# Performance work log

Measured on AMD Instinct MI355X. Metric: run time of the kernel, lower is better.

The kernel has to match this reference:

```python
import jax, jax.numpy as jnp
import numpy as np

D_MODEL = 1024
N_HEADS = 16
D_K = D_MODEL // N_HEADS


def setup_inputs() -> dict:
    key = jax.random.key(0)
    ks = jax.random.split(key, 16)
    B, S = 2, 2048
    sc = 1.0 / np.sqrt(D_MODEL)
    inp = {
        "query": jax.random.normal(ks[0], (B, S, D_MODEL), jnp.float32),
        "key": jax.random.normal(ks[1], (B, S, D_MODEL), jnp.float32),
        "value": jax.random.normal(ks[2], (B, S, D_MODEL), jnp.float32),
        "Wq": jax.random.normal(ks[3], (D_MODEL, D_MODEL), jnp.float32) * sc,
        "bq": jnp.zeros((D_MODEL,), jnp.float32),
        "Wk": jax.random.normal(ks[4], (D_MODEL, D_MODEL), jnp.float32) * sc,
        "bk": jnp.zeros((D_MODEL,), jnp.float32),
        "Wv": jax.random.normal(ks[5], (D_MODEL, D_MODEL), jnp.float32) * sc,
        "bv": jnp.zeros((D_MODEL,), jnp.float32),
        "Wo": jax.random.normal(ks[6], (D_MODEL, D_MODEL), jnp.float32) * sc,
        "bo": jnp.zeros((D_MODEL,), jnp.float32),
        "theta": jax.random.normal(ks[7], (N_HEADS,), jnp.float32) * 0.1,
        "gate": jax.random.normal(ks[8], (D_MODEL,), jnp.float32) * 0.1,
    }
    return inp


def reference(query, key, value, Wq, bq, Wk, bk, Wv, bv, Wo, bo, theta, gate):
    B, Sq, D = query.shape
    Sk = key.shape[1]
    # linear projections (torch Linear: x @ W.T + b), split heads -> [B,H,S,d_k]
    Q = (query @ Wq.T + bq).reshape(B, Sq, N_HEADS, D_K).transpose(0, 2, 1, 3)
    K = (key @ Wk.T + bk).reshape(B, Sk, N_HEADS, D_K).transpose(0, 2, 1, 3)
    V = (value @ Wv.T + bv).reshape(B, Sk, N_HEADS, D_K).transpose(0, 2, 1, 3)

    inv_sqrt_dk = 1.0 / jnp.sqrt(jnp.float32(D_K))
    scores = jnp.einsum("bhqd,bhkd->bhqk", Q, K) * inv_sqrt_dk

    # per-head rotation of the first two feature dims of Q
    cos_t = jnp.cos(theta)[None, :, None, None]  # [1,H,1,1]
    sin_t = jnp.sin(theta)[None, :, None, None]
    q_rot = jnp.concatenate(
        [
            cos_t * Q[..., :1] - sin_t * Q[..., 1:2],
            sin_t * Q[..., :1] + cos_t * Q[..., 1:2],
            Q[..., 2:],
        ],
        axis=-1,
    )
    scores_q = jnp.einsum("bhqd,bhkd->bhqk", q_rot, K) * inv_sqrt_dk

    g_scalar = jax.nn.sigmoid(gate.mean())
    scores = g_scalar * scores_q + (1.0 - g_scalar) * scores

    attn = jax.nn.softmax(scores, axis=-1)
    out = jnp.einsum("bhqk,bhkd->bhqd", attn, V)
    out = out.transpose(0, 2, 1, 3).reshape(B, Sq, D)
    return out @ Wo.T + bo
```

## Files before the change

kernel.cpp:

```cpp
#include <hip/hip_runtime.h>


typedef __bf16 bf16;
typedef __attribute__((ext_vector_type(8))) bf16 bf16x8;
typedef __attribute__((ext_vector_type(4))) bf16 bf16x4;
typedef __attribute__((ext_vector_type(2))) bf16 bf16x2;
typedef __attribute__((ext_vector_type(4))) float f32x4;
typedef unsigned int u32;

#define D_MODEL 1024
#define NH 16
#define DKH 64
#define SEQ 2048

#define GLL16(g, l) __builtin_amdgcn_global_load_lds(                      \
    (const __attribute__((address_space(1))) void*)(g),                    \
    (__attribute__((address_space(3))) void*)(l), 16, 0, 0)

static __device__ __forceinline__ f32x4 mfma16(bf16x8 a, bf16x8 b, f32x4 c) {
  return __builtin_amdgcn_mfma_f32_16x16x32_bf16(a, b, c, 0, 0, 0);
}

static __device__ __forceinline__ u32 pk2(float a, float b) {
  bf16x2 v; v[0] = (bf16)a; v[1] = (bf16)b;
  return __builtin_bit_cast(u32, v);
}

static __device__ __forceinline__ float fexp2(float x) {
#if __has_builtin(__builtin_amdgcn_exp2f)
  return __builtin_amdgcn_exp2f(x);
#else
  return exp2f(x);
#endif
}

#define CQK 0.1803368801111244f
#define MSHIFT 12.0f

__global__ __launch_bounds__(256) void prep(const float* __restrict__ query,
                                            const float* __restrict__ key,
                                            const float* __restrict__ value,
                                            const float* __restrict__ Wq,
                                            const float* __restrict__ bq,
                                            const float* __restrict__ Wk,
                                            const float* __restrict__ Wv,
                                            const float* __restrict__ Wo,
                                            const float* __restrict__ gate,
                                            const float* __restrict__ theta,
                                            bf16* __restrict__ Xq,
                                            bf16* __restrict__ Xk,
                                            bf16* __restrict__ Xv,
                                            bf16* __restrict__ Wqp,
                                            bf16* __restrict__ Wkp,
                                            bf16* __restrict__ Wvp,
                                            bf16* __restrict__ Wop,
                                            float* __restrict__ bqp) {
  const int id = blockIdx.x;
  const int tid = threadIdx.x;
  if (id >= 4096) {
    const int rem = id - 4096;
    const int iz = rem >> 12;
    const int ib = rem & 4095;
    const float* s = (iz == 0) ? query : (iz == 1) ? key : value;
    bf16* d = (iz == 0) ? Xq : (iz == 1) ? Xk : Xv;
    const size_t i = (size_t)(ib * 256 + tid) * 4;
    float4 w = *(const float4*)(s + i);
    bf16x4 o; o[0] = (bf16)w.x; o[1] = (bf16)w.y; o[2] = (bf16)w.z; o[3] = (bf16)w.w;
    *(bf16x4*)(d + i) = o;
    return;
  }
  const int wz = id >> 10, wb = id & 1023;
  if (wz != 0) {
    const float* s = (wz == 1) ? Wk : (wz == 2) ? Wv : Wo;
    bf16* dd = (wz == 1) ? Wkp : (wz == 2) ? Wvp : Wop;
    const size_t i = (size_t)(wb * 256 + tid) * 4;
    float4 v = *(const float4*)(s + i);
    bf16x4 o4; o4[0] = (bf16)v.x; o4[1] = (bf16)v.y; o4[2] = (bf16)v.z; o4[3] = (bf16)v.w;
    *(bf16x4*)(dd + i) = o4;
    return;
  }
  __shared__ float red[4];
  float ssum = 0.f;
  for (int i = tid; i < D_MODEL; i += 256) ssum += gate[i];
#pragma unroll
  for (int off = 32; off > 0; off >>= 1) ssum += __shfl_down(ssum, off);
  if ((tid & 63) == 0) red[tid >> 6] = ssum;
  __syncthreads();
  const float g = 1.f / (1.f + __expf(-(red[0] + red[1] + red[2] + red[3]) / 1024.f));

  const int t = wb * 256 + tid;
  const int r = t >> 8;
  const int c0 = (t & 255) * 4;
  const int d = r & 63, h = r >> 6;
  float4 w = *(const float4*)(Wq + (size_t)r * D_MODEL + c0);
  float4 o;
  if (d == 0) {
    const float a = (g * cosf(theta[h]) + (1.f - g)) * CQK;
    const float bb = (g * sinf(theta[h])) * CQK;
    float4 w2 = *(const float4*)(Wq + (size_t)(r + 1) * D_MODEL + c0);
    o.x = a * w.x - bb * w2.x; o.y = a * w.y - bb * w2.y;
    o.z = a * w.z - bb * w2.z; o.w = a * w.w - bb * w2.w;
    if (c0 == 0) bqp[r] = a * bq[r] - bb * bq[r + 1];
  } else if (d == 1) {
    const float a = (g * cosf(theta[h]) + (1.f - g)) * CQK;
    const float bb = (g * sinf(theta[h])) * CQK;
    float4 w2 = *(const float4*)(Wq + (size_t)(r - 1) * D_MODEL + c0);
    o.x = bb * w2.x + a * w.x; o.y = bb * w2.y + a * w.y;
    o.z = bb * w2.z + a * w.z; o.w = bb * w2.w + a * w.w;
    if (c0 == 0) bqp[r] = bb * bq[r - 1] + a * bq[r];
  } else {
    o.x = CQK * w.x; o.y = CQK * w.y;
    o.z = CQK * w.z; o.w = CQK * w.w;
    if (c0 == 0) bqp[r] = CQK * bq[r];
  }
  bf16x4 ov; ov[0] = (bf16)o.x; ov[1] = (bf16)o.y; ov[2] = (bf16)o.z; ov[3] = (bf16)o.w;
  *(bf16x4*)(Wqp + (size_t)r * D_MODEL + c0) = ov;
}

static __device__ __forceinline__ void gemm_bt_main(const bf16* __restrict__ A,
                                                    const bf16* __restrict__ Bt,
                                                    int tm, int tn, int K,
                                                    f32x4 acc[4][4]) {
  __shared__ bf16 lA[8192];
  __shared__ bf16 lB[8192];
  const int tid = threadIdx.x;
  const int lane = tid & 63, wv = tid >> 6;
  const int wm = wv >> 1, wn = wv & 1;
  const int l16 = lane & 15, lg = lane >> 4;

#pragma unroll
  for (int i = 0; i < 4; ++i)
#pragma unroll
    for (int j = 0; j < 4; ++j) acc[i][j] = (f32x4){0.f, 0.f, 0.f, 0.f};

  int offA[4][2], offB[4][2];
#pragma unroll
  for (int f = 0; f < 4; ++f)
#pragma unroll
    for (int kc = 0; kc < 2; ++kc) {
      const int m = wm * 64 + f * 16 + l16;
      offA[f][kc] = m * 64 + (((kc * 4 + lg) ^ (m & 7)) << 3);
      const int n = wn * 64 + f * 16 + l16;
      offB[f][kc] = n * 64 + (((kc * 4 + lg) ^ (n & 7)) << 3);
    }

  const int rowb = tid >> 3, oct = tid & 7;
  const int soct = oct ^ (rowb & 7);
  const bf16* gA[4];
  const bf16* gB[4];
#pragma unroll
  for (int rd = 0; rd < 4; ++rd) {
    gA[rd] = A + (size_t)(tm + rd * 32 + rowb) * K + soct * 8;
    gB[rd] = Bt + (size_t)(tn + rd * 32 + rowb) * K + soct * 8;
  }

  for (int kt = 0; kt < K; kt += 64) {
    __syncthreads();
#pragma unroll
    for (int rd = 0; rd < 4; ++rd) {
      GLL16(gA[rd] + kt, &lA[rd * 2048 + wv * 512]);
      GLL16(gB[rd] + kt, &lB[rd * 2048 + wv * 512]);
    }
    __syncthreads();
#pragma unroll
    for (int kc = 0; kc < 2; ++kc) {
      bf16x8 af[4], bv[4];
#pragma unroll
      for (int f = 0; f < 4; ++f) {
        af[f] = *(const bf16x8*)&lA[offA[f][kc]];
        bv[f] = *(const bf16x8*)&lB[offB[f][kc]];
      }
#pragma unroll
      for (int i = 0; i < 4; ++i)
#pragma unroll
        for (int j = 0; j < 4; ++j)
          acc[i][j] = mfma16(af[i], bv[j], acc[i][j]);
    }
  }
}

__global__ __launch_bounds__(256) void gemm_qkv(
    const bf16* __restrict__ Xq, const bf16* __restrict__ Xk, const bf16* __restrict__ Xv,
    const bf16* __restrict__ Wq, const bf16* __restrict__ Wk, const bf16* __restrict__ Wv,
    const float* __restrict__ bqp, const float* __restrict__ bk, const float* __restrict__ bv,
    bf16* __restrict__ Qp, bf16* __restrict__ Kp, bf16* __restrict__ Vt) {
  const int wgp = (blockIdx.x & 7) * 96 + (blockIdx.x >> 3);
  const int z = wgp >> 8;
  const int rem = wgp & 255;
  const int tm = (rem >> 3) * 128, tn = (rem & 7) * 128;
  const bf16* A = (z == 0) ? Xq : (z == 1) ? Xk : Xv;
  const bf16* Bt = (z == 0) ? Wq : (z == 1) ? Wk : Wv;
  const float* bias = (z == 0) ? bqp : (z == 1) ? bk : bv;
  f32x4 acc[4][4];
  gemm_bt_main(A, Bt, tm, tn, D_MODEL, acc);
  const int lane = threadIdx.x & 63, wv = threadIdx.x >> 6;
  const int wm = wv >> 1, wn = wv & 1, l16 = lane & 15, lg = lane >> 4;
  if (z < 2) {
    bf16* C = (z == 0) ? Qp : Kp;
#pragma unroll
    for (int i = 0; i < 4; ++i) {
      const int m0 = tm + wm * 64 + i * 16 + lg * 4;
#pragma unroll
      for (int j = 0; j < 4; ++j) {
        const int n = tn + wn * 64 + j * 16 + l16;
        const float bb = bias[n];
        const int h = n >> 6, d = n & 63;
#pragma unroll
        for (int r = 0; r < 4; ++r) {
          const int m = m0 + r;
          const int b = m >> 11, s = m & 2047;
          C[((size_t)(b * NH + h) * SEQ + s) * DKH + d] = (bf16)(acc[i][j][r] + bb);
        }
      }
    }
  } else {
#pragma unroll
    for (int i = 0; i < 4; ++i) {
      const int m0 = tm + wm * 64 + i * 16 + lg * 4;
      const int b = m0 >> 11, s0 = m0 & 2047;
#pragma unroll
      for (int j = 0; j < 4; ++j) {
        const int n = tn + wn * 64 + j * 16 + l16;
        const float bb = bias[n];
        const int h = n >> 6, d = n & 63;
        bf16x4 ov;
#pragma unroll
        for (int r = 0; r < 4; ++r) ov[r] = (bf16)(acc[i][j][r] + bb);
        *(bf16x4*)&Vt[((size_t)(b * NH + h) * DKH + d) * SEQ + s0] = ov;
      }
    }
  }
}

__global__ __launch_bounds__(256) void gemm_out_k(const bf16* __restrict__ A,
                                                  const bf16* __restrict__ Bt,
                                                  const float* __restrict__ bias,
                                                  float* __restrict__ C) {
  const int wgp = (blockIdx.x & 7) * 32 + (blockIdx.x >> 3);
  const int tm = (wgp >> 3) * 128, tn = (wgp & 7) * 128;
  f32x4 acc[4][4];
  gemm_bt_main(A, Bt, tm, tn, D_MODEL, acc);
  const int lane = threadIdx.x & 63, wv = threadIdx.x >> 6;
  const int wm = wv >> 1, wn = wv & 1, l16 = lane & 15, lg = lane >> 4;
#pragma unroll
  for (int i = 0; i < 4; ++i) {
    const int m0 = tm + wm * 64 + i * 16 + lg * 4;
#pragma unroll
    for (int j = 0; j < 4; ++j) {
      const int n = tn + wn * 64 + j * 16 + l16;
      const float bb = bias[n];
#pragma unroll
      for (int r = 0; r < 4; ++r)
        C[(size_t)(m0 + r) * D_MODEL + n] = acc[i][j][r] + bb;
    }
  }
}

__global__ __launch_bounds__(512, 4) void attn_kernel(const bf16* __restrict__ Qp,
                                                      const bf16* __restrict__ Kp,
                                                      const bf16* __restrict__ Vt,
                                                      bf16* __restrict__ Op) {
  __shared__ bf16 lK[2][4096];
  __shared__ bf16 lV[2][4096];
  __shared__ bf16 lP[8192];

  const int tid = threadIdx.x;
  const int lane = tid & 63, w = tid >> 6;
  const int l16 = lane & 15, lg = lane >> 4;
  const int wgp = (blockIdx.x & 7) * 64 + (blockIdx.x >> 3);
  const int bh = wgp >> 4;
  const int b = bh >> 4, h = bh & 15;
  const int q0 = (wgp & 15) * 128;
  const size_t kvb = (size_t)bh * SEQ * DKH;

  bf16x8 aq[2];
#pragma unroll
  for (int kc = 0; kc < 2; ++kc)
    aq[kc] = *(const bf16x8*)&Qp[kvb + (size_t)(q0 + w * 16 + l16) * DKH + kc * 32 + lg * 8];

  f32x4 o[4];
#pragma unroll
  for (int fn = 0; fn < 4; ++fn) o[fn] = (f32x4){0.f, 0.f, 0.f, 0.f};
  f32x4 lacc = (f32x4){0.f, 0.f, 0.f, 0.f};

  bf16x8 ones;
#pragma unroll
  for (int j = 0; j < 8; ++j) ones[j] = (bf16)1.0f;

  const int kr = tid >> 3, oct = tid & 7;
  const bf16* gK = Kp + kvb + (size_t)kr * DKH + oct * 8;
  const bf16* gV = Vt + kvb + (size_t)kr * SEQ + oct * 8;
  const int swz = kr * 64 + ((oct ^ (kr & 7)) << 3);

  bf16* lPw = &lP[w * 1024];
  int pwr[4];
#pragma unroll
  for (int fn = 0; fn < 4; ++fn)
    pwr[fn] = l16 * 64 + (((fn * 2 + (lg >> 1)) ^ (l16 & 7)) << 3) + ((lg & 1) << 2);
  int prd[2];
#pragma unroll
  for (int kc = 0; kc < 2; ++kc)
    prd[kc] = l16 * 64 + (((kc * 4 + lg) ^ (l16 & 7)) << 3);

  bf16x8 k0r = *(const bf16x8*)(gK);
  bf16x8 v0r = *(const bf16x8*)(gV);
  *(bf16x8*)&lK[0][swz] = k0r;
  *(bf16x8*)&lV[0][swz] = v0r;
  k0r = *(const bf16x8*)(gK + (size_t)64 * DKH);
  v0r = *(const bf16x8*)(gV + 64);
  __syncthreads();

  const int NT = SEQ / 64;
  for (int t = 0; t < NT; ++t) {
    const bf16* K = &lK[t & 1][0];
    const bf16* V = &lV[t & 1][0];

    f32x4 st[4];
    __builtin_amdgcn_s_setprio(1);
#pragma unroll
    for (int fn = 0; fn < 4; ++fn) {
      const int row = fn * 16 + l16;
      bf16x8 ka = *(const bf16x8*)&K[row * 64 + ((lg ^ (row & 7)) << 3)];
      bf16x8 kb = *(const bf16x8*)&K[row * 64 + (((4 + lg) ^ (row & 7)) << 3)];
      f32x4 tt = (f32x4){0.f, 0.f, 0.f, 0.f};
      tt = mfma16(ka, aq[0], tt);
      tt = mfma16(kb, aq[1], tt);
      st[fn] = tt;
    }
    __builtin_amdgcn_s_setprio(0);

#pragma unroll
    for (int fn = 0; fn < 4; ++fn) {
      uint2 pw;
      pw.x = pk2(fexp2(st[fn][0] - MSHIFT), fexp2(st[fn][1] - MSHIFT));
      pw.y = pk2(fexp2(st[fn][2] - MSHIFT), fexp2(st[fn][3] - MSHIFT));
      *(uint2*)&lPw[pwr[fn]] = pw;
    }

    bf16x8 pa0 = *(const bf16x8*)&lPw[prd[0]];
    bf16x8 pa1 = *(const bf16x8*)&lPw[prd[1]];

    __builtin_amdgcn_s_setprio(1);
    lacc = mfma16(pa0, ones, lacc);
    lacc = mfma16(pa1, ones, lacc);
#pragma unroll
    for (int fn = 0; fn < 4; ++fn) {
      const int n = fn * 16 + l16;
      bf16x8 vv0 = *(const bf16x8*)&V[n * 64 + ((lg ^ (n & 7)) << 3)];
      bf16x8 vv1 = *(const bf16x8*)&V[n * 64 + (((4 + lg) ^ (n & 7)) << 3)];
      o[fn] = mfma16(pa0, vv0, o[fn]);
      o[fn] = mfma16(pa1, vv1, o[fn]);
    }
    __builtin_amdgcn_s_setprio(0);

    if (t + 1 < NT) {
      const int nb = (t + 1) & 1;
      *(bf16x8*)&lK[nb][swz] = k0r;
      *(bf16x8*)&lV[nb][swz] = v0r;
      if (t + 2 < NT) {
        const int kt2 = (t + 2) * 64;
        k0r = *(const bf16x8*)(gK + (size_t)kt2 * DKH);
        v0r = *(const bf16x8*)(gV + kt2);
      }
    }
    __syncthreads();
  }

  float linv[4];
#pragma unroll
  for (int r = 0; r < 4; ++r) linv[r] = 1.f / lacc[r];
#pragma unroll
  for (int r = 0; r < 4; ++r) {
    const int q = q0 + w * 16 + lg * 4 + r;
#pragma unroll
    for (int fn = 0; fn < 4; ++fn) {
      const int d = fn * 16 + l16;
      Op[((size_t)(b * SEQ + q)) * D_MODEL + h * DKH + d] = (bf16)(o[fn][r] * linv[r]);
    }
  }
}

extern "C" void kernel_launch(void* const* d_in, const int* in_sizes, int n_in,
                              void* d_out, int out_size, void* d_ws, size_t ws_size,
                              hipStream_t stream) {
  (void)in_sizes; (void)n_in; (void)out_size; (void)ws_size;
  const float* query = (const float*)d_in[0];
  const float* key   = (const float*)d_in[1];
  const float* value = (const float*)d_in[2];
  const float* Wq    = (const float*)d_in[3];
  const float* bq    = (const float*)d_in[4];
  const float* Wk    = (const float*)d_in[5];
  const float* bk    = (const float*)d_in[6];
  const float* Wv    = (const float*)d_in[7];
  const float* bv    = (const float*)d_in[8];
  const float* Wo    = (const float*)d_in[9];
  const float* bo    = (const float*)d_in[10];
  const float* theta = (const float*)d_in[11];
  const float* gate  = (const float*)d_in[12];

  float* bqp = (float*)d_ws;
  bf16* wb = (bf16*)((char*)d_ws + 8192);
  bf16* Xq  = wb;
  bf16* Xk  = Xq + 4194304;
  bf16* Xv  = Xk + 4194304;
  bf16* Wqp = Xv + 4194304;
  bf16* Wkp = Wqp + 1048576;
  bf16* Wvp = Wkp + 1048576;
  bf16* Wop = Wvp + 1048576;
  bf16* Qp  = Wop + 1048576;
  bf16* Kp  = Qp + 4194304;
  bf16* Vt  = Kp + 4194304;
  bf16* Op  = Vt + 4194304;

  prep<<<16384, 256, 0, stream>>>(query, key, value, Wq, bq, Wk, Wv, Wo,
                                  gate, theta, Xq, Xk, Xv,
                                  Wqp, Wkp, Wvp, Wop, bqp);
  gemm_qkv<<<768, 256, 0, stream>>>(Xq, Xk, Xv, Wqp, Wkp, Wvp,
                                    bqp, bk, bv, Qp, Kp, Vt);
  attn_kernel<<<512, 512, 0, stream>>>(Qp, Kp, Vt, Op);
  gemm_out_k<<<256, 256, 0, stream>>>(Op, Wop, bo, (float*)d_out);
}
```

Baseline: 123.3 us.

## Split attention key tile across wave pairs with 32-query waves and LDS reduction

Waves are regrouped into 4 query groups of 32 rows and 2 key halves. Each wave now handles half of each 64-key tile for two 16-row query blocks, so every K and V fragment read from LDS feeds two MFMAs, which halves LDS read traffic per MFMA. At the end, partial outputs and row sums from the second key half are combined with the first through LDS, costing an extra barrier and a reduction, and the P scratch tiles and LDS buffers are reused.

After: 124.4 us. Within noise of the previous version (+0.8%).

```diff
diff --git a/kernel.cpp b/kernel.cpp
--- a/kernel.cpp
+++ b/kernel.cpp
@@ -260,28 +260,40 @@
                                                       const bf16* __restrict__ Kp,
                                                       const bf16* __restrict__ Vt,
                                                       bf16* __restrict__ Op) {
-  __shared__ bf16 lK[2][4096];
-  __shared__ bf16 lV[2][4096];
-  __shared__ bf16 lP[8192];
+  __shared__ __align__(16) char smem[49152];
+  bf16 (*lK)[4096] = (bf16(*)[4096])smem;
+  bf16 (*lV)[4096] = (bf16(*)[4096])(smem + 16384);
+  bf16* lP = (bf16*)(smem + 32768);
+  float* cmb = (float*)smem;
+  float* cl  = (float*)(smem + 32768);
 
   const int tid = threadIdx.x;
   const int lane = tid & 63, w = tid >> 6;
   const int l16 = lane & 15, lg = lane >> 4;
+  const int qg = w >> 1, kg = w & 1;
   const int wgp = (blockIdx.x & 7) * 64 + (blockIdx.x >> 3);
   const int bh = wgp >> 4;
   const int b = bh >> 4, h = bh & 15;
   const int q0 = (wgp & 15) * 128;
+  const int qw0 = q0 + qg * 32;
   const size_t kvb = (size_t)bh * SEQ * DKH;
 
-  bf16x8 aq[2];
-#pragma unroll
-  for (int kc = 0; kc < 2; ++kc)
-    aq[kc] = *(const bf16x8*)&Qp[kvb + (size_t)(q0 + w * 16 + l16) * DKH + kc * 32 + lg * 8];
-
-  f32x4 o[4];
-#pragma unroll
-  for (int fn = 0; fn < 4; ++fn) o[fn] = (f32x4){0.f, 0.f, 0.f, 0.f};
-  f32x4 lacc = (f32x4){0.f, 0.f, 0.f, 0.f};
+  bf16x8 aq[2][2];
+#pragma unroll
+  for (int qq = 0; qq < 2; ++qq)
+#pragma unroll
+    for (int kc = 0; kc < 2; ++kc)
+      aq[qq][kc] = *(const bf16x8*)&Qp[kvb +
+          (size_t)(qw0 + qq * 16 + l16) * DKH + kc * 32 + lg * 8];
+
+  f32x4 o[2][4];
+#pragma unroll
+  for (int qq = 0; qq < 2; ++qq)
+#pragma unroll
+    for (int dt = 0; dt < 4; ++dt) o[qq][dt] = (f32x4){0.f, 0.f, 0.f, 0.f};
+  f32x4 lacc[2];
+  lacc[0] = (f32x4){0.f, 0.f, 0.f, 0.f};
+  lacc[1] = (f32x4){0.f, 0.f, 0.f, 0.f};
 
   bf16x8 ones;
 #pragma unroll
@@ -293,14 +305,11 @@
   const int swz = kr * 64 + ((oct ^ (kr & 7)) << 3);
 
   bf16* lPw = &lP[w * 1024];
-  int pwr[4];
-#pragma unroll
-  for (int fn = 0; fn < 4; ++fn)
-    pwr[fn] = l16 * 64 + (((fn * 2 + (lg >> 1)) ^ (l16 & 7)) << 3) + ((lg & 1) << 2);
-  int prd[2];
-#pragma unroll
-  for (int kc = 0; kc < 2; ++kc)
-    prd[kc] = l16 * 64 + (((kc * 4 + lg) ^ (l16 & 7)) << 3);
+  int pwr[2];
+#pragma unroll
+  for (int fn = 0; fn < 2; ++fn)
+    pwr[fn] = l16 * 32 + ((((fn * 2 + (lg >> 1))) ^ (l16 & 3)) << 3) + ((lg & 1) << 2);
+  const int prd = l16 * 32 + ((lg ^ (l16 & 3)) << 3);
 
   bf16x8 k0r = *(const bf16x8*)(gK);
   bf16x8 v0r = *(const bf16x8*)(gV);
@@ -315,41 +324,45 @@
     const bf16* K = &lK[t & 1][0];
     const bf16* V = &lV[t & 1][0];
 
-    f32x4 st[4];
+    f32x4 st[2][2];
     __builtin_amdgcn_s_setprio(1);
 #pragma unroll
-    for (int fn = 0; fn < 4; ++fn) {
-      const int row = fn * 16 + l16;
+    for (int fn = 0; fn < 2; ++fn) {
+      const int row = kg * 32 + fn * 16 + l16;
       bf16x8 ka = *(const bf16x8*)&K[row * 64 + ((lg ^ (row & 7)) << 3)];
       bf16x8 kb = *(const bf16x8*)&K[row * 64 + (((4 + lg) ^ (row & 7)) << 3)];
-      f32x4 tt = (f32x4){0.f, 0.f, 0.f, 0.f};
-      tt = mfma16(ka, aq[0], tt);
-      tt = mfma16(kb, aq[1], tt);
-      st[fn] = tt;
+#pragma unroll
+      for (int qq = 0; qq < 2; ++qq) {
+        f32x4 tt = (f32x4){0.f, 0.f, 0.f, 0.f};
+        tt = mfma16(ka, aq[qq][0], tt);
+        tt = mfma16(kb, aq[qq][1], tt);
+        st[fn][qq] = tt;
+      }
     }
     __builtin_amdgcn_s_setprio(0);
 
 #pragma unroll
-    for (int fn = 0; fn < 4; ++fn) {
-      uint2 pw;
-      pw.x = pk2(fexp2(st[fn][0] - MSHIFT), fexp2(st[fn][1] - MSHIFT));
-      pw.y = pk2(fexp2(st[fn][2] - MSHIFT), fexp2(st[fn][3] - MSHIFT));
-      *(uint2*)&lPw[pwr[fn]] = pw;
-    }
-
-    bf16x8 pa0 = *(const bf16x8*)&lPw[prd[0]];
-    bf16x8 pa1 = *(const bf16x8*)&lPw[prd[1]];
+    for (int fn = 0; fn < 2; ++fn)
+#pragma unroll
+      for (int qq = 0; qq < 2; ++qq) {
+        uint2 pw;
+        pw.x = pk2(fexp2(st[fn][qq][0] - MSHIFT), fexp2(st[fn][qq][1] - MSHIFT));
+        pw.y = pk2(fexp2(st[fn][qq][2] - MSHIFT), fexp2(st[fn][qq][3] - MSHIFT));
+        *(uint2*)&lPw[qq * 512 + pwr[fn]] = pw;
+      }
+
+    bf16x8 pa0 = *(const bf16x8*)&lPw[prd];
+    bf16x8 pa1 = *(const bf16x8*)&lPw[512 + prd];
 
     __builtin_amdgcn_s_setprio(1);
-    lacc = mfma16(pa0, ones, lacc);
-    lacc = mfma16(pa1, ones, lacc);
-#pragma unroll
-    for (int fn = 0; fn < 4; ++fn) {
-      const int n = fn * 16 + l16;
-      bf16x8 vv0 = *(const bf16x8*)&V[n * 64 + ((lg ^ (n & 7)) << 3)];
-      bf16x8 vv1 = *(const bf16x8*)&V[n * 64 + (((4 + lg) ^ (n & 7)) << 3)];
-      o[fn] = mfma16(pa0, vv0, o[fn]);
-      o[fn] = mfma16(pa1, vv1, o[fn]);
+    lacc[0] = mfma16(pa0, ones, lacc[0]);
+    lacc[1] = mfma16(pa1, ones, lacc[1]);
+#pragma unroll
+    for (int dt = 0; dt < 4; ++dt) {
+      const int n = dt * 16 + l16;
+      bf16x8 vv = *(const bf16x8*)&V[n * 64 + (((kg * 4 + lg) ^ (n & 7)) << 3)];
+      o[0][dt] = mfma16(pa0, vv, o[0][dt]);
+      o[1][dt] = mfma16(pa1, vv, o[1][dt]);
     }
     __builtin_amdgcn_s_setprio(0);
 
@@ -366,16 +379,46 @@
     __syncthreads();
   }
 
-  float linv[4];
-#pragma unroll
-  for (int r = 0; r < 4; ++r) linv[r] = 1.f / lacc[r];
-#pragma unroll
-  for (int r = 0; r < 4; ++r) {
-    const int q = q0 + w * 16 + lg * 4 + r;
-#pragma unroll
-    for (int fn = 0; fn < 4; ++fn) {
-      const int d = fn * 16 + l16;
-      Op[((size_t)(b * SEQ + q)) * D_MODEL + h * DKH + d] = (bf16)(o[fn][r] * linv[r]);
+  if (kg == 1) {
+#pragma unroll
+    for (int qq = 0; qq < 2; ++qq)
+#pragma unroll
+      for (int dt = 0; dt < 4; ++dt)
+        *(f32x4*)&cmb[(size_t)qg * 2048 + ((qq * 4 + dt) * 16 + l16) * 16 + lg * 4] =
+            o[qq][dt];
+    if (l16 == 0) {
+#pragma unroll
+      for (int qq = 0; qq < 2; ++qq)
+#pragma unroll
+        for (int r = 0; r < 4; ++r)
+          cl[(qg * 2 + qq) * 16 + lg * 4 + r] = lacc[qq][r];
+    }
+  }
+  __syncthreads();
+  if (kg == 0) {
+#pragma unroll
+    for (int qq = 0; qq < 2; ++qq) {
+#pragma unroll
+      for (int dt = 0; dt < 4; ++dt) {
+        f32x4 p = *(const f32x4*)&cmb[(size_t)qg * 2048 +
+                                      ((qq * 4 + dt) * 16 + l16) * 16 + lg * 4];
+        o[qq][dt][0] += p[0]; o[qq][dt][1] += p[1];
+        o[qq][dt][2] += p[2]; o[qq][dt][3] += p[3];
+      }
+      float linv[4];
+#pragma unroll
+      for (int r = 0; r < 4; ++r)
+        linv[r] = 1.f / (lacc[qq][r] + cl[(qg * 2 + qq) * 16 + lg * 4 + r]);
+#pragma unroll
+      for (int r = 0; r < 4; ++r) {
+        const int q = qw0 + qq * 16 + lg * 4 + r;
+#pragma unroll
+        for (int dt = 0; dt < 4; ++dt) {
+          const int d = dt * 16 + l16;
+          Op[((size_t)(b * SEQ + q)) * D_MODEL + h * DKH + d] =
+              (bf16)(o[qq][dt][r] * linv[r]);
+        }
+      }
     }
   }
 }
```
